# Kernel optimization log

Measured on AMD Instinct MI355X. Metric: run time of the kernel, lower is better.

The kernel has to match this reference:

```python
import jax, jax.numpy as jnp
import numpy as np

B, GRID, WIDTH, NBLOCKS = 128, 32, 100, 50  # num_layers=100 -> 50 two-GEMM residual blocks


def _forward(inputs, W0, Wa, Wb, b1, b2, b3, b4, mult, Wout, bout):
    Bb, G = inputs.shape[0], inputs.shape[1]
    T = G // 2
    even = jnp.arange(0, G, 2)
    odd = even + 1
    idx = (even - 1) % G  # [(i-1) % G for even i]

    def patch(i1, i2):
        # gather axis1 then axis2 -> (B, T, T, 3, 3) flattened to (B*T*T, 9)
        return inputs[:, i1][:, :, i2].reshape(-1, 9)

    # order: right, left, up, down, center (matches tf.concat order)
    flat = jnp.concatenate([patch(odd, even), patch(idx, even), patch(even, odd),
                            patch(even, idx), patch(even, even)], axis=-1)  # (B*T*T, 45)

    x = jax.nn.relu(flat @ W0)  # (B*T*T, 100)

    def block(x, p):
        wa, wb, bb1, bb2, bb3, bb4, m = p
        x1 = (x + bb1) @ wa
        x1 = 2.0 * x1 + bb2          # x1 + bias_2 + x1
        x1 = jax.nn.relu(x1)
        x1 = 2.0 * x1 + bb3          # x1 + bias_3 + x1
        x1 = (x1 @ wb) * m
        x = jax.nn.relu(x + x1 + bb4)
        return x, None

    x, _ = jax.lax.scan(block, x, (Wa, Wb, b1, b2, b3, b4, mult))

    x = (x @ Wout + bout).reshape(Bb, T, T, 4)

    jp1 = (jnp.arange(T) + 1) % T
    jm1 = (jnp.arange(T) - 1) % T
    x0, x1c, x2, x3 = x[..., 0], x[..., 1], x[..., 2], x[..., 3]
    right_c = x0 / (x1c[:, jp1] + x0)
    left_c = x1c / (x1c + x0[:, jm1])
    up_c = x2 / (x2 + x3[:, :, jp1])
    down_c = x3 / (x2[:, :, jm1] + x3)

    # corner contributions from the original fine-grid stencils
    oo = inputs[:, odd][:, :, odd]    # odd-odd fine points (ru corner)
    oi = inputs[:, odd][:, :, idx]    # rd corner
    io = inputs[:, idx][:, :, odd]    # lu corner
    ii = inputs[:, idx][:, :, idx]    # ld corner
    ru = -(oo[..., 0, 0] + oo[..., 1, 0] * right_c + oo[..., 0, 1] * up_c) / oo[..., 1, 1]
    rd = -(oi[..., 0, 2] + oi[..., 1, 2] * right_c + oi[..., 0, 1] * down_c) / oi[..., 1, 1]
    lu = -(io[..., 2, 0] + io[..., 1, 0] * left_c + io[..., 2, 1] * up_c) / io[..., 1, 1]
    ld = -(ii[..., 2, 2] + ii[..., 1, 2] * left_c + ii[..., 2, 1] * down_c) / ii[..., 1, 1]

    ones = jnp.ones_like(down_c)
    first_row = jnp.stack([ld, left_c, lu], axis=-1)
    second_row = jnp.stack([down_c, ones, up_c], axis=-1)
    third_row = jnp.stack([rd, right_c, ru], axis=-1)
    out = jnp.stack([first_row, second_row, third_row], axis=0)  # (3, B, T, T, 3)
    return jnp.transpose(out, (1, 2, 3, 0, 4))  # (B, T, T, 3, 3)


def setup_inputs() -> dict:
    key = jax.random.key(0)
    ks = jax.random.split(key, 6)
    # positive stencil entries keep the corner divisions well-conditioned
    inputs = jax.random.uniform(ks[0], (B, GRID, GRID, 3, 3), jnp.float32) + 0.5
    W0 = jax.random.normal(ks[1], (45, WIDTH), jnp.float32) * np.float32(np.sqrt(2.0 / 45))
    Wa = jax.random.normal(ks[2], (NBLOCKS, WIDTH, WIDTH), jnp.float32) * np.float32(np.sqrt(2.0 / WIDTH))
    # original inits linear_{i+1} to zeros; small random keeps the baseline non-degenerate
    Wb = jax.random.normal(ks[3], (NBLOCKS, WIDTH, WIDTH), jnp.float32) * np.float32(0.01)
    b1 = jnp.zeros((NBLOCKS,), jnp.float32)
    b2 = jnp.zeros((NBLOCKS,), jnp.float32)
    b3 = jnp.zeros((NBLOCKS,), jnp.float32)
    b4 = jnp.zeros((NBLOCKS,), jnp.float32)
    mult = jnp.ones((NBLOCKS,), jnp.float32)
    Wout = jax.random.normal(ks[4], (WIDTH, 4), jnp.float32) * np.float32(0.05)
    bout = jnp.ones((4,), jnp.float32)  # keeps contribution denominators ~2 (stable)
    return {"inputs": inputs, "W0": W0, "Wa": Wa, "Wb": Wb, "b1": b1, "b2": b2,
            "b3": b3, "b4": b4, "mult": mult, "Wout": Wout, "bout": bout}


def reference(inputs, W0, Wa, Wb, b1, b2, b3, b4, mult, Wout, bout):
    return _forward(inputs, W0, Wa, Wb, b1, b2, b3, b4, mult, Wout, bout)
```

## Files before the change

kernel.cpp:

```cpp
#include <hip/hip_runtime.h>
#include <cstddef>

typedef _Float16 f16x8 __attribute__((ext_vector_type(8)));
typedef _Float16 f16x4 __attribute__((ext_vector_type(4)));
typedef float f32x4 __attribute__((ext_vector_type(4)));
typedef float f32x16 __attribute__((ext_vector_type(16)));

constexpr int BATCH = 128;
constexpr int T     = 16;
constexpr int ROWS  = BATCH * T * T;
constexpr int WID   = 100;
constexpr int NB    = 50;
constexpr int KP    = 128;
constexpr int KS    = 7;
constexpr int NP    = 128;
constexpr int RPW   = 64;
constexpr int WCH   = KS * 4 * 512;

__global__ __launch_bounds__(256) void prep_kernel(
    const float* __restrict__ Wa, const float* __restrict__ Wb,
    _Float16* __restrict__ whi, _Float16* __restrict__ wlo,
    float* __restrict__ csA) {
  const int bid = blockIdx.x;
  const int bk = bid >> 1, m = bid & 1;
  const float* src = (m ? Wb : Wa) + (size_t)bk * (WID * WID);
  _Float16* dh = whi + (size_t)bid * WCH;
  _Float16* dl = wlo + (size_t)bid * WCH;
  for (int e = threadIdx.x; e < WCH; e += 256) {
    const int i  = e & 7;
    const int L  = (e >> 3) & 63;
    const int ct = (e >> 9) & 3;
    const int ks = e >> 11;
    const int k  = 16 * ks + 8 * (L >> 5) + i;
    const int j  = 32 * ct + (L & 31);
    const float v = (k < WID && j < WID) ? src[k * WID + j] : 0.0f;
    const _Float16 hi = (_Float16)v;
    dh[e] = hi;
    dl[e] = (_Float16)(v - (float)hi);
  }
  if (!m) {
    for (int col = threadIdx.x; col < NP; col += 256) {
      float s = 0.0f;
      if (col < WID) {
        for (int k = 0; k < WID; ++k) s += src[k * WID + col];
      }
      csA[bk * NP + col] = s;
    }
  }
}

__global__ __launch_bounds__(256) void first_layer_kernel(
    const float* __restrict__ inp, const float* __restrict__ W0,
    float* __restrict__ x0) {
  __shared__ float w0s[45 * WID];
  for (int i = threadIdx.x; i < 45 * WID; i += 256) w0s[i] = W0[i];
  __syncthreads();

  const int rq  = threadIdx.x >> 2;
  const int cq  = threadIdx.x & 3;
  const int row = blockIdx.x * 64 + rq;
  const int b   = row >> 8;
  const int t1  = (row >> 4) & 15;
  const int t2  = row & 15;
  const int g1  = 2 * t1, g2 = 2 * t2;
  const int g1m = (g1 + 31) & 31, g2m = (g2 + 31) & 31;
  const float* base = inp + (size_t)b * (32 * 32 * 9);
  const float* p0 = base + ((g1 + 1) * 32 + g2) * 9;
  const float* p1 = base + (g1m * 32 + g2) * 9;
  const float* p2 = base + (g1 * 32 + (g2 + 1)) * 9;
  const float* p3 = base + (g1 * 32 + g2m) * 9;
  const float* p4 = base + (g1 * 32 + g2) * 9;

  float f[45];
#pragma unroll
  for (int qq = 0; qq < 9; ++qq) {
    f[qq]      = p0[qq];
    f[9 + qq]  = p1[qq];
    f[18 + qq] = p2[qq];
    f[27 + qq] = p3[qq];
    f[36 + qq] = p4[qq];
  }

  float acc[25];
#pragma unroll
  for (int j = 0; j < 25; ++j) acc[j] = 0.0f;
  const int j0 = cq * 25;
#pragma unroll
  for (int k = 0; k < 45; ++k) {
    const float fv = f[k];
#pragma unroll
    for (int j = 0; j < 25; ++j) acc[j] += fv * w0s[k * WID + j0 + j];
  }
  float* orow = x0 + (size_t)row * WID + j0;
#pragma unroll
  for (int j = 0; j < 25; ++j) orow[j] = fmaxf(acc[j], 0.0f);
}

__global__ __launch_bounds__(512, 2) void chain_kernel(
    float* __restrict__ x0,
    const _Float16* __restrict__ whi, const _Float16* __restrict__ wlo,
    const float* __restrict__ csA,
    const float* __restrict__ B1, const float* __restrict__ B2,
    const float* __restrict__ B3, const float* __restrict__ B4,
    const float* __restrict__ M) {
  __shared__ __align__(16) _Float16 xhs[RPW * KP];
  __shared__ __align__(16) _Float16 xls[RPW * KP];
  __shared__ __align__(16) _Float16 vhs[RPW * KP];
  __shared__ __align__(16) _Float16 vls[RPW * KP];

  const int tid  = threadIdx.x;
  const int lane = tid & 63;
  const int uw   = __builtin_amdgcn_readfirstlane(tid >> 6);
  const int rt   = uw >> 2;
  const int ct   = uw & 3;
  const int jr   = lane & 31;
  const int kg   = lane >> 5;
  const int rbase = blockIdx.x * RPW;

  const int row_x = 32 * rt + jr;
  const int sw    = (row_x & 15) << 3;

  for (int i = tid; i < RPW * KP; i += 512) {
    const int row = i >> 7, k = i & 127;
    const float v = (k < WID) ? x0[(size_t)(rbase + row) * WID + k] : 0.0f;
    const _Float16 hi = (_Float16)v;
    const int a = row * KP + (k ^ ((row & 15) << 3));
    xhs[a] = hi;
    xls[a] = (_Float16)(v - (float)hi);
  }

  int j0g[4];
#pragma unroll
  for (int g = 0; g < 4; ++g) j0g[g] = 32 * ct + 4 * kg + 8 * g;

  f32x4 xres[4];
#pragma unroll
  for (int g = 0; g < 4; ++g) {
    if (j0g[g] <= WID - 4) {
      xres[g] = *(const f32x4*)&x0[(size_t)(rbase + row_x) * WID + j0g[g]];
    } else {
      xres[g] = (f32x4){0.f, 0.f, 0.f, 0.f};
    }
  }
  __syncthreads();

  f32x16 acc;

  auto kloop = [&](const int gidx,
                   const _Float16* __restrict__ xhsrc,
                   const _Float16* __restrict__ xlsrc) {
    const _Float16* gh = whi + (size_t)gidx * WCH + ct * 512;
    const _Float16* gl = wlo + (size_t)gidx * WCH + ct * 512;
    f16x8 wh[KS], wl[KS];
#pragma unroll
    for (int ks = 0; ks < KS; ++ks) {
      wh[ks] = *(const f16x8*)&gh[ks * 2048 + lane * 8];
      wl[ks] = *(const f16x8*)&gl[ks * 2048 + lane * 8];
    }
#pragma unroll
    for (int ks = 0; ks < KS; ++ks) {
      const int off = row_x * KP + ((16 * ks + 8 * kg) ^ sw);
      const f16x8 xh = *(const f16x8*)&xhsrc[off];
      const f16x8 xl = *(const f16x8*)&xlsrc[off];
      acc = __builtin_amdgcn_mfma_f32_32x32x16_f16(wh[ks], xh, acc, 0, 0, 0);
      acc = __builtin_amdgcn_mfma_f32_32x32x16_f16(wl[ks], xh, acc, 0, 0, 0);
      acc = __builtin_amdgcn_mfma_f32_32x32x16_f16(wh[ks], xl, acc, 0, 0, 0);
    }
  };

  for (int bk = 0; bk < NB; ++bk) {
#pragma unroll
    for (int e = 0; e < 16; ++e) acc[e] = 0.0f;
    kloop(bk * 2, xhs, xls);
    {
      const float b1 = B1[bk], b2 = B2[bk], b3 = B3[bk];
#pragma unroll
      for (int g = 0; g < 4; ++g) {
        const f32x4 cs = *(const f32x4*)&csA[bk * NP + j0g[g]];
        f16x4 hv, lv;
#pragma unroll
        for (int r = 0; r < 4; ++r) {
          const float t = 2.0f * (acc[g * 4 + r] + b1 * cs[r]) + b2;
          const float v = 2.0f * fmaxf(t, 0.0f) + b3;
          const _Float16 hi = (_Float16)v;
          hv[r] = hi;
          lv[r] = (_Float16)(v - (float)hi);
        }
        const int a = row_x * KP + (j0g[g] ^ sw);
        *(f16x4*)&vhs[a] = hv;
        *(f16x4*)&vls[a] = lv;
      }
    }
    __syncthreads();

#pragma unroll
    for (int e = 0; e < 16; ++e) acc[e] = 0.0f;
    kloop(bk * 2 + 1, vhs, vls);
    {
      const float b4v = B4[bk], mm = M[bk];
#pragma unroll
      for (int g = 0; g < 4; ++g) {
        f16x4 hv, lv;
#pragma unroll
        for (int r = 0; r < 4; ++r) {
          const float xn = fmaxf(xres[g][r] + acc[g * 4 + r] * mm + b4v, 0.0f);
          xres[g][r] = xn;
          const _Float16 hi = (_Float16)xn;
          hv[r] = hi;
          lv[r] = (_Float16)(xn - (float)hi);
        }
        const int a = row_x * KP + (j0g[g] ^ sw);
        *(f16x4*)&xhs[a] = hv;
        *(f16x4*)&xls[a] = lv;
      }
    }
    __syncthreads();
  }

#pragma unroll
  for (int g = 0; g < 4; ++g) {
    if (j0g[g] <= WID - 4)
      *(f32x4*)&x0[(size_t)(rbase + row_x) * WID + j0g[g]] = xres[g];
  }
}

__global__ __launch_bounds__(256) void out_kernel(
    const float* __restrict__ inp, const float* __restrict__ x0,
    const float* __restrict__ Wout, const float* __restrict__ bout,
    float* __restrict__ out) {
  __shared__ float ys[256 * 4];
  __shared__ float wouts[WID * 4];
  __shared__ float bos[4];
  const int tid = threadIdx.x;
  const int b   = blockIdx.x;

  for (int i = tid; i < WID * 4; i += 256) wouts[i] = Wout[i];
  if (tid < 4) bos[tid] = bout[tid];
  __syncthreads();

  const int row = b * 256 + tid;
  const float* xr = x0 + (size_t)row * WID;
  float a0 = 0.f, a1 = 0.f, a2 = 0.f, a3 = 0.f;
#pragma unroll 4
  for (int k = 0; k < WID; ++k) {
    const float xv = xr[k];
    a0 += xv * wouts[k * 4 + 0];
    a1 += xv * wouts[k * 4 + 1];
    a2 += xv * wouts[k * 4 + 2];
    a3 += xv * wouts[k * 4 + 3];
  }
  ys[tid * 4 + 0] = a0 + bos[0];
  ys[tid * 4 + 1] = a1 + bos[1];
  ys[tid * 4 + 2] = a2 + bos[2];
  ys[tid * 4 + 3] = a3 + bos[3];
  __syncthreads();

  const int i = tid >> 4, j = tid & 15;
  const int ip1 = (i + 1) & 15, im1 = (i + 15) & 15;
  const int jp1 = (j + 1) & 15, jm1 = (j + 15) & 15;
  auto Y = [&](int a, int c, int comp) { return ys[(((a << 4) | c) << 2) + comp]; };
  const float y0 = Y(i, j, 0), y1 = Y(i, j, 1), y2 = Y(i, j, 2), y3 = Y(i, j, 3);
  const float right_c = y0 / (Y(ip1, j, 1) + y0);
  const float left_c  = y1 / (y1 + Y(im1, j, 0));
  const float up_c    = y2 / (y2 + Y(i, jp1, 3));
  const float down_c  = y3 / (Y(i, jm1, 2) + y3);

  const float* base = inp + (size_t)b * (32 * 32 * 9);
  const int g1 = 2 * i + 1, g1m = (2 * i + 31) & 31;
  const int g2 = 2 * j + 1, g2m = (2 * j + 31) & 31;
  const float* oo = base + (g1 * 32 + g2) * 9;
  const float* oi = base + (g1 * 32 + g2m) * 9;
  const float* io = base + (g1m * 32 + g2) * 9;
  const float* ii = base + (g1m * 32 + g2m) * 9;
  const float ru = -(oo[0] + oo[3] * right_c + oo[1] * up_c) / oo[4];
  const float rd = -(oi[2] + oi[5] * right_c + oi[1] * down_c) / oi[4];
  const float lu = -(io[6] + io[3] * left_c + io[7] * up_c) / io[4];
  const float ld = -(ii[8] + ii[5] * left_c + ii[7] * down_c) / ii[4];

  float* o = out + (size_t)row * 9;
  o[0] = ld;     o[1] = left_c;  o[2] = lu;
  o[3] = down_c; o[4] = 1.0f;    o[5] = up_c;
  o[6] = rd;     o[7] = right_c; o[8] = ru;
}

extern "C" void kernel_launch(void* const* d_in, const int* in_sizes, int n_in,
                              void* d_out, int out_size, void* d_ws, size_t ws_size,
                              hipStream_t stream) {
  const float* inp  = (const float*)d_in[0];
  const float* W0   = (const float*)d_in[1];
  const float* Wa   = (const float*)d_in[2];
  const float* Wb   = (const float*)d_in[3];
  const float* B1   = (const float*)d_in[4];
  const float* B2   = (const float*)d_in[5];
  const float* B3   = (const float*)d_in[6];
  const float* B4   = (const float*)d_in[7];
  const float* M    = (const float*)d_in[8];
  const float* Wout = (const float*)d_in[9];
  const float* bout = (const float*)d_in[10];
  float* out = (float*)d_out;

  float* ws     = (float*)d_ws;
  float* x0     = ws;
  _Float16* whi = (_Float16*)(ws + 3276800);
  _Float16* wlo = (_Float16*)(ws + 3276800 + 716800);
  float* csA    = ws + 3276800 + 716800 + 716800;

  hipLaunchKernelGGL(prep_kernel, dim3(100), dim3(256), 0, stream,
                     Wa, Wb, whi, wlo, csA);
  hipLaunchKernelGGL(first_layer_kernel, dim3(ROWS / 64), dim3(256), 0, stream,
                     inp, W0, x0);
  hipLaunchKernelGGL(chain_kernel, dim3(ROWS / RPW), dim3(512), 0, stream,
                     x0, whi, wlo, csA, B1, B2, B3, B4, M);
  hipLaunchKernelGGL(out_kernel, dim3(BATCH), dim3(256), 0, stream,
                     inp, x0, Wout, bout, out);
}
```

Before: 328.3 us.

## Prefetch next GEMM weights across barriers and fold per-block biases into precomputed vectors

```diff
diff --git a/kernel.cpp b/kernel.cpp
--- a/kernel.cpp
+++ b/kernel.cpp
@@ -3,6 +3,7 @@
 
 typedef _Float16 f16x8 __attribute__((ext_vector_type(8)));
 typedef _Float16 f16x4 __attribute__((ext_vector_type(4)));
+typedef __fp16 h16x2 __attribute__((ext_vector_type(2)));
 typedef float f32x4 __attribute__((ext_vector_type(4)));
 typedef float f32x16 __attribute__((ext_vector_type(16)));
 
@@ -19,8 +20,11 @@
 
 __global__ __launch_bounds__(256) void prep_kernel(
     const float* __restrict__ Wa, const float* __restrict__ Wb,
+    const float* __restrict__ B1, const float* __restrict__ B2,
+    const float* __restrict__ B3, const float* __restrict__ B4,
+    const float* __restrict__ M,
     _Float16* __restrict__ whi, _Float16* __restrict__ wlo,
-    float* __restrict__ csA) {
+    float* __restrict__ c1, float* __restrict__ c2, float* __restrict__ S) {
   const int bid = blockIdx.x;
   const int bk = bid >> 1, m = bid & 1;
   const float* src = (m ? Wb : Wa) + (size_t)bk * (WID * WID);
@@ -38,15 +42,18 @@
     dh[e] = hi;
     dl[e] = (_Float16)(v - (float)hi);
   }
-  if (!m) {
-    for (int col = threadIdx.x; col < NP; col += 256) {
-      float s = 0.0f;
-      if (col < WID) {
-        for (int k = 0; k < WID; ++k) s += src[k * WID + col];
-      }
-      csA[bk * NP + col] = s;
-    }
-  }
+  for (int col = threadIdx.x; col < NP; col += 256) {
+    float s = 0.0f;
+    if (col < WID) {
+      for (int k = 0; k < WID; ++k) s += src[k * WID + col];
+    }
+    if (!m) {
+      c1[bk * NP + col] = B1[bk] * s + 0.5f * B2[bk];
+    } else {
+      c2[bk * NP + col] = M[bk] * B3[bk] * s + B4[bk];
+    }
+  }
+  if (!m && threadIdx.x == 0) S[bk] = 4.0f * M[bk];
 }
 
 __global__ __launch_bounds__(256) void first_layer_kernel(
@@ -99,10 +106,8 @@
 __global__ __launch_bounds__(512, 2) void chain_kernel(
     float* __restrict__ x0,
     const _Float16* __restrict__ whi, const _Float16* __restrict__ wlo,
-    const float* __restrict__ csA,
-    const float* __restrict__ B1, const float* __restrict__ B2,
-    const float* __restrict__ B3, const float* __restrict__ B4,
-    const float* __restrict__ M) {
+    const float* __restrict__ c1, const float* __restrict__ c2,
+    const float* __restrict__ S) {
   __shared__ __align__(16) _Float16 xhs[RPW * KP];
   __shared__ __align__(16) _Float16 xls[RPW * KP];
   __shared__ __align__(16) _Float16 vhs[RPW * KP];
@@ -120,6 +125,19 @@
   const int row_x = 32 * rt + jr;
   const int sw    = (row_x & 15) << 3;
 
+  f16x8 wh[KS], wl[KS];
+  auto load_w = [&](const int gidx) {
+    const _Float16* gh = whi + (size_t)gidx * WCH + ct * 512;
+    const _Float16* gl = wlo + (size_t)gidx * WCH + ct * 512;
+#pragma unroll
+    for (int ks = 0; ks < KS; ++ks) {
+      wh[ks] = *(const f16x8*)&gh[ks * 2048 + lane * 8];
+      wl[ks] = *(const f16x8*)&gl[ks * 2048 + lane * 8];
+    }
+  };
+
+  load_w(0);
+
   for (int i = tid; i < RPW * KP; i += 512) {
     const int row = i >> 7, k = i & 127;
     const float v = (k < WID) ? x0[(size_t)(rbase + row) * WID + k] : 0.0f;
@@ -146,17 +164,8 @@
 
   f32x16 acc;
 
-  auto kloop = [&](const int gidx,
-                   const _Float16* __restrict__ xhsrc,
+  auto kloop = [&](const _Float16* __restrict__ xhsrc,
                    const _Float16* __restrict__ xlsrc) {
-    const _Float16* gh = whi + (size_t)gidx * WCH + ct * 512;
-    const _Float16* gl = wlo + (size_t)gidx * WCH + ct * 512;
-    f16x8 wh[KS], wl[KS];
-#pragma unroll
-    for (int ks = 0; ks < KS; ++ks) {
-      wh[ks] = *(const f16x8*)&gh[ks * 2048 + lane * 8];
-      wl[ks] = *(const f16x8*)&gl[ks * 2048 + lane * 8];
-    }
 #pragma unroll
     for (int ks = 0; ks < KS; ++ks) {
       const int off = row_x * KP + ((16 * ks + 8 * kg) ^ sw);
@@ -171,47 +180,54 @@
   for (int bk = 0; bk < NB; ++bk) {
 #pragma unroll
     for (int e = 0; e < 16; ++e) acc[e] = 0.0f;
-    kloop(bk * 2, xhs, xls);
+    kloop(xhs, xls);
+    load_w(bk * 2 + 1);
+#pragma unroll
+    for (int g = 0; g < 4; ++g) {
+      const f32x4 c1v = *(const f32x4*)&c1[bk * NP + j0g[g]];
+      float u0 = fmaxf(acc[g * 4 + 0] + c1v[0], 0.0f);
+      float u1 = fmaxf(acc[g * 4 + 1] + c1v[1], 0.0f);
+      float u2 = fmaxf(acc[g * 4 + 2] + c1v[2], 0.0f);
+      float u3 = fmaxf(acc[g * 4 + 3] + c1v[3], 0.0f);
+      const h16x2 h01 = __builtin_amdgcn_cvt_pkrtz(u0, u1);
+      const h16x2 h23 = __builtin_amdgcn_cvt_pkrtz(u2, u3);
+      const h16x2 l01 = __builtin_amdgcn_cvt_pkrtz(u0 - (float)h01[0],
+                                                   u1 - (float)h01[1]);
+      const h16x2 l23 = __builtin_amdgcn_cvt_pkrtz(u2 - (float)h23[0],
+                                                   u3 - (float)h23[1]);
+      const int a = row_x * KP + (j0g[g] ^ sw);
+      *(h16x2*)&vhs[a]     = h01;
+      *(h16x2*)&vhs[a + 2] = h23;
+      *(h16x2*)&vls[a]     = l01;
+      *(h16x2*)&vls[a + 2] = l23;
+    }
+    __syncthreads();
+
+#pragma unroll
+    for (int e = 0; e < 16; ++e) acc[e] = 0.0f;
+    kloop(vhs, vls);
+    load_w(bk + 1 < NB ? bk * 2 + 2 : 0);
     {
-      const float b1 = B1[bk], b2 = B2[bk], b3 = B3[bk];
+      const float s = S[bk];
 #pragma unroll
       for (int g = 0; g < 4; ++g) {
-        const f32x4 cs = *(const f32x4*)&csA[bk * NP + j0g[g]];
-        f16x4 hv, lv;
-#pragma unroll
-        for (int r = 0; r < 4; ++r) {
-          const float t = 2.0f * (acc[g * 4 + r] + b1 * cs[r]) + b2;
-          const float v = 2.0f * fmaxf(t, 0.0f) + b3;
-          const _Float16 hi = (_Float16)v;
-          hv[r] = hi;
-          lv[r] = (_Float16)(v - (float)hi);
-        }
+        const f32x4 c2v = *(const f32x4*)&c2[bk * NP + j0g[g]];
+        float n0 = fmaxf(xres[g][0] + fmaf(acc[g * 4 + 0], s, c2v[0]), 0.0f);
+        float n1 = fmaxf(xres[g][1] + fmaf(acc[g * 4 + 1], s, c2v[1]), 0.0f);
+        float n2 = fmaxf(xres[g][2] + fmaf(acc[g * 4 + 2], s, c2v[2]), 0.0f);
+        float n3 = fmaxf(xres[g][3] + fmaf(acc[g * 4 + 3], s, c2v[3]), 0.0f);
+        xres[g][0] = n0; xres[g][1] = n1; xres[g][2] = n2; xres[g][3] = n3;
+        const h16x2 h01 = __builtin_amdgcn_cvt_pkrtz(n0, n1);
+        const h16x2 h23 = __builtin_amdgcn_cvt_pkrtz(n2, n3);
+        const h16x2 l01 = __builtin_amdgcn_cvt_pkrtz(n0 - (float)h01[0],
+                                                     n1 - (float)h01[1]);
+        const h16x2 l23 = __builtin_amdgcn_cvt_pkrtz(n2 - (float)h23[0],
+                                                     n3 - (float)h23[1]);
         const int a = row_x * KP + (j0g[g] ^ sw);
-        *(f16x4*)&vhs[a] = hv;
-        *(f16x4*)&vls[a] = lv;
-      }
-    }
-    __syncthreads();
-
-#pragma unroll
-    for (int e = 0; e < 16; ++e) acc[e] = 0.0f;
-    kloop(bk * 2 + 1, vhs, vls);
-    {
-      const float b4v = B4[bk], mm = M[bk];
-#pragma unroll
-      for (int g = 0; g < 4; ++g) {
-        f16x4 hv, lv;
-#pragma unroll
-        for (int r = 0; r < 4; ++r) {
-          const float xn = fmaxf(xres[g][r] + acc[g * 4 + r] * mm + b4v, 0.0f);
-          xres[g][r] = xn;
-          const _Float16 hi = (_Float16)xn;
-          hv[r] = hi;
-          lv[r] = (_Float16)(xn - (float)hi);
-        }
-        const int a = row_x * KP + (j0g[g] ^ sw);
-        *(f16x4*)&xhs[a] = hv;
-        *(f16x4*)&xls[a] = lv;
+        *(h16x2*)&xhs[a]     = h01;
+        *(h16x2*)&xhs[a + 2] = h23;
+        *(h16x2*)&xls[a]     = l01;
+        *(h16x2*)&xls[a + 2] = l23;
       }
     }
     __syncthreads();
@@ -303,14 +319,16 @@
   float* x0     = ws;
   _Float16* whi = (_Float16*)(ws + 3276800);
   _Float16* wlo = (_Float16*)(ws + 3276800 + 716800);
-  float* csA    = ws + 3276800 + 716800 + 716800;
+  float* c1     = ws + 3276800 + 716800 + 716800;
+  float* c2     = c1 + 6400;
+  float* S      = c2 + 6400;
 
   hipLaunchKernelGGL(prep_kernel, dim3(100), dim3(256), 0, stream,
-                     Wa, Wb, whi, wlo, csA);
+                     Wa, Wb, B1, B2, B3, B4, M, whi, wlo, c1, c2, S);
   hipLaunchKernelGGL(first_layer_kernel, dim3(ROWS / 64), dim3(256), 0, stream,
                      inp, W0, x0);
   hipLaunchKernelGGL(chain_kernel, dim3(ROWS / RPW), dim3(512), 0, stream,
-                     x0, whi, wlo, csA, B1, B2, B3, B4, M);
+                     x0, whi, wlo, c1, c2, S);
   hipLaunchKernelGGL(out_kernel, dim3(BATCH), dim3(256), 0, stream,
                      inp, x0, Wout, bout, out);
 }
```

Measured after the change: 398.9 us. 21.5% more time.
